# Performance work log

Hardware: AMD Instinct MI355X
Metric: run time of the kernel (lower is better)

The kernel has to match this reference:

```python
import jax, jax.numpy as jnp
import numpy as np

IN_OUT_DIM = 1024
HALF = IN_OUT_DIM // 2  # 512
MID = 4096
HIDDEN = 4
BATCH = 8192


def _mlp(h, Ws, bs):
    # Linear+ReLU for all but last layer, plain Linear at the end.
    for W, b in zip(Ws[:-1], bs[:-1]):
        h = jax.nn.relu(h @ W + b)
    return h @ Ws[-1] + bs[-1]


def setup_inputs() -> dict:
    key = jax.random.key(0)
    ks = jax.random.split(key, 16)
    inp = {
        "x": jax.random.normal(ks[0], (BATCH, IN_OUT_DIM), dtype=jnp.float32),
        "log_det_J": jnp.zeros((1,), dtype=jnp.float32),
    }
    dims = [HALF] + [MID] * (HIDDEN + 1) + [HALF]
    # Layers: 512->4096, (4096->4096) x4, 4096->512  => 6 Linear layers
    for i in range(len(dims) - 1):
        fan_in = dims[i]
        scale = 1.0 / np.sqrt(fan_in)
        inp[f"W{i}"] = jax.random.uniform(ks[1 + 2 * i], (dims[i], dims[i + 1]), jnp.float32, -scale, scale)
        inp[f"b{i}"] = jax.random.uniform(ks[2 + 2 * i], (dims[i + 1],), jnp.float32, -scale, scale)
    return inp


def reference(x, log_det_J, W0, b0, W1, b1, W2, b2, W3, b3, W4, b4, W5, b5):
    Ws = [W0, W1, W2, W3, W4, W5]
    bs = [b0, b1, b2, b3, b4, b5]
    # split_channels_even_odd: even cols 0,2,4..., odd cols 1,3,5...
    even = x[:, 0::2]  # [B, HALF]
    odd = x[:, 1::2]   # [B, HALF]
    # mask_config=1: transform even using MLP(odd), keep odd. reverse=False -> add.
    transformed = even + _mlp(odd, Ws, bs)
    kept = odd
    # stack_data with mask_config=1: columns [t0, k0, t1, k1, ...]
    B = x.shape[0]
    stacked = jnp.stack([transformed, kept], axis=2).reshape(B, -1)
    return stacked, log_det_J
```

## Files before the change

kernel.cpp:

```cpp
#include <hip/hip_runtime.h>
#include <hip/hip_bf16.h>
#include <hip/hip_fp16.h>


typedef __attribute__((ext_vector_type(8))) _Float16 f16x8;
typedef __attribute__((ext_vector_type(4))) float    f32x4;
typedef __attribute__((ext_vector_type(4))) int      i32x4;

#define B_ROWS 8192
#define D_HALF 512
#define D_MID  4096

__device__ __forceinline__ void gld_lds16(const void* gptr, void* lptr) {
    __builtin_amdgcn_global_load_lds(
        (const __attribute__((address_space(1))) void*)gptr,
        (__attribute__((address_space(3))) void*)lptr,
        16, 0, 0);
}

__device__ __forceinline__ void amax_commit(float m, int lane, float* amax_out) {
#pragma unroll
    for (int off = 32; off > 0; off >>= 1)
        m = fmaxf(m, __shfl_down(m, off));
    if (lane == 0) atomicMax((unsigned int*)amax_out, __float_as_uint(m));
}

__global__ __launch_bounds__(256) void transpose_convert_f16(
    const float* __restrict__ src, __half* __restrict__ dst, int K, int N)
{
    __shared__ float tile[32][33];
    const int kt = blockIdx.y * 32, nt = blockIdx.x * 32;
    const int tx = threadIdx.x, ty = threadIdx.y;
#pragma unroll
    for (int i = 0; i < 32; i += 8)
        tile[ty + i][tx] = src[(size_t)(kt + ty + i) * N + nt + tx];
    __syncthreads();
#pragma unroll
    for (int i = 0; i < 32; i += 8)
        dst[(size_t)(nt + ty + i) * K + kt + tx] = __float2half(tile[tx][ty + i]);
}

__global__ __launch_bounds__(256) void transpose_convert_i8(
    const float* __restrict__ src, signed char* __restrict__ dst, int K, int N)
{
    __shared__ float tile[32][33];
    const int kt = blockIdx.y * 32, nt = blockIdx.x * 32;
    const int tx = threadIdx.x, ty = threadIdx.y;
#pragma unroll
    for (int i = 0; i < 32; i += 8)
        tile[ty + i][tx] = src[(size_t)(kt + ty + i) * N + nt + tx];
    __syncthreads();
#pragma unroll
    for (int i = 0; i < 32; i += 8) {
        int q = __float2int_rn(tile[tx][ty + i] * 8128.0f);
        q = q > 127 ? 127 : (q < -127 ? -127 : q);
        dst[(size_t)(nt + ty + i) * K + kt + tx] = (signed char)q;
    }
}

__global__ __launch_bounds__(256) void extract_odd(
    const float* __restrict__ x, __half* __restrict__ odd,
    const float* __restrict__ ldj, float* __restrict__ out)
{
    const int idx = blockIdx.x * 256 + threadIdx.x;
    const float2 v = ((const float2*)x)[idx];
    odd[idx] = __float2half(v.y);
    if (idx == 0) out[(size_t)B_ROWS * 1024] = ldj[0];
}

__global__ __launch_bounds__(256) void quantize_i8(
    const __half* __restrict__ h, const float* __restrict__ amaxp,
    signed char* __restrict__ q)
{
    const int idx = blockIdx.x * 256 + threadIdx.x;
    const float inv = 127.0f / amaxp[0];
    const f16x8 v = ((const f16x8*)h)[idx];
    int p0 = 0, p1 = 0;
#pragma unroll
    for (int k = 0; k < 4; k++) {
        int a = __float2int_rn((float)v[k] * inv);
        a = a > 127 ? 127 : a;
        p0 |= a << (8 * k);
    }
#pragma unroll
    for (int k = 0; k < 4; k++) {
        int a = __float2int_rn((float)v[4 + k] * inv);
        a = a > 127 ? 127 : a;
        p1 |= a << (8 * k);
    }
    ((int2*)q)[idx] = make_int2(p0, p1);
}

template <int MODE>
__global__ __launch_bounds__(256, 2) void gemm_f16(
    const __half* __restrict__ A, const __half* __restrict__ Bt,
    const float* __restrict__ bias,
    __half* __restrict__ Ch, const float* __restrict__ xin,
    float* __restrict__ outp, float* __restrict__ amax_out,
    int M, int N, int K)
{
    __shared__ __half sA[128 * 32];
    __shared__ __half sB[128 * 32];

    const int tid  = threadIdx.x;
    const int wave = tid >> 6;
    const int lane = tid & 63;
    const int wm = wave >> 1, wn = wave & 1;
    const int quad = lane >> 4, l16 = lane & 15;
    const int bm = blockIdx.y, bn = blockIdx.x;

    const int    srow   = wave * 16 + (lane >> 2);
    const int    schunk = ((lane & 3) - ((lane >> 3) & 3)) & 3;
    const size_t ldb    = (size_t)K * 2;

    const char* Ag = (const char*)A  + (size_t)(bm * 128 + srow) * ldb + schunk * 16;
    const char* Bg = (const char*)Bt + (size_t)(bn * 128 + srow) * ldb + schunk * 16;
    char* sA0 = (char*)sA + wave * 16 * 64;
    char* sB0 = (char*)sB + wave * 16 * 64;

    const int pc = (quad + ((l16 >> 1) & 3)) & 3;
    const __half* aBase = sA + (wm * 64 + l16) * 32 + pc * 8;
    const __half* bBase = sB + (wn * 64 + l16) * 32 + pc * 8;

    f32x4 acc[4][4] = {};

    for (int k0 = 0; k0 < K; k0 += 32) {
        __syncthreads();
        const size_t kb = (size_t)k0 * 2;
        gld_lds16(Ag + kb,            sA0);
        gld_lds16(Ag + 64 * ldb + kb, sA0 + 64 * 64);
        gld_lds16(Bg + kb,            sB0);
        gld_lds16(Bg + 64 * ldb + kb, sB0 + 64 * 64);
        __syncthreads();

        f16x8 a[4], b[4];
#pragma unroll
        for (int i = 0; i < 4; i++) a[i] = *(const f16x8*)(aBase + i * 16 * 32);
#pragma unroll
        for (int j = 0; j < 4; j++) b[j] = *(const f16x8*)(bBase + j * 16 * 32);
#pragma unroll
        for (int i = 0; i < 4; i++)
#pragma unroll
            for (int j = 0; j < 4; j++)
                acc[i][j] = __builtin_amdgcn_mfma_f32_16x16x32_f16(a[i], b[j], acc[i][j], 0, 0, 0);
    }

    const int m0 = bm * 128 + wm * 64;
    const int n0 = bn * 128 + wn * 64;
    float lmax = 0.0f;
#pragma unroll
    for (int j = 0; j < 4; j++) {
        const int n  = n0 + j * 16 + l16;
        const float bv = bias[n];
#pragma unroll
        for (int i = 0; i < 4; i++) {
            const int mb = m0 + i * 16 + quad * 4;
#pragma unroll
            for (int r = 0; r < 4; r++) {
                float v = acc[i][j][r] + bv;
                if (MODE == 0) {
                    v = v > 0.0f ? v : 0.0f;
                    lmax = fmaxf(lmax, v);
                    Ch[(size_t)(mb + r) * N + n] = __float2half(v);
                } else {
                    const size_t p = (size_t)(mb + r) * 512 + n;
                    const float2 xv = ((const float2*)xin)[p];
                    float2 o; o.x = xv.x + v; o.y = xv.y;
                    ((float2*)outp)[p] = o;
                }
            }
        }
    }
    if (MODE == 0) amax_commit(lmax, lane, amax_out);
}

__global__ __launch_bounds__(512, 2) void gemm_i8_256(
    const signed char* __restrict__ A, const signed char* __restrict__ Bt,
    const float* __restrict__ bias, const float* __restrict__ amaxp,
    __half* __restrict__ Ch, float* __restrict__ amax_out,
    int M, int N, int K)
{
    __shared__ __align__(16) signed char lds[131072];

    const int tid  = threadIdx.x;
    const int wave = tid >> 6;
    const int lane = tid & 63;
    const int wm = wave >> 2, wn = wave & 3;
    const int quad = lane >> 4, l16 = lane & 15;
    const int bm = blockIdx.y, bn = blockIdx.x;

    const int srow   = tid >> 2;
    const int schunk = ((tid & 3) - ((tid >> 3) & 3)) & 3;
    const signed char* Ag = A  + (size_t)(bm * 256 + srow) * K + schunk * 16;
    const signed char* Bg = Bt + (size_t)(bn * 256 + srow) * K + schunk * 16;

    signed char* ldsA = lds;
    signed char* ldsB = lds + 65536;
    const int woff = wave * 1024;

    const int pc = (quad + ((l16 >> 1) & 3)) & 3;
    const signed char* aB = ldsA + (wm * 128 + l16) * 64 + pc * 16;
    const signed char* bB = ldsB + (wn * 64  + l16) * 64 + pc * 16;

    i32x4 acc[8][4] = {};
    const int NT = K >> 6;

#define STAGE_A(TT) { const size_t kb = (size_t)(TT) * 64;                       \
        signed char* d = ldsA + ((TT) & 3) * 16384 + woff;                        \
        gld_lds16(Ag + kb, d); gld_lds16(Ag + (size_t)128 * K + kb, d + 8192); }
#define STAGE_B(TT) { const size_t kb = (size_t)(TT) * 64;                       \
        signed char* d = ldsB + ((TT) & 3) * 16384 + woff;                        \
        gld_lds16(Bg + kb, d); gld_lds16(Bg + (size_t)128 * K + kb, d + 8192); }

    STAGE_A(0); STAGE_B(0);
    STAGE_A(1); STAGE_B(1);
    STAGE_A(2); STAGE_B(2);

    for (int t = 0; t < NT; ++t) {
        const signed char* aT = aB + (t & 3) * 16384;
        const signed char* bT = bB + (t & 3) * 16384;

        if (t < NT - 2)       asm volatile("s_waitcnt vmcnt(8)" ::: "memory");
        else if (t == NT - 2) asm volatile("s_waitcnt vmcnt(4)" ::: "memory");
        else                  asm volatile("s_waitcnt vmcnt(0)" ::: "memory");
        __builtin_amdgcn_s_barrier();

        i32x4 a[4], b[4];
#pragma unroll
        for (int j = 0; j < 4; j++) b[j] = *(const i32x4*)(bT + j * 16 * 64);
#pragma unroll
        for (int i = 0; i < 4; i++) a[i] = *(const i32x4*)(aT + i * 16 * 64);
        if (t + 3 < NT) STAGE_A(t + 3);
        __builtin_amdgcn_s_barrier();
        __builtin_amdgcn_s_setprio(1);
#pragma unroll
        for (int i = 0; i < 4; i++)
#pragma unroll
            for (int j = 0; j < 4; j++)
                acc[i][j] = __builtin_amdgcn_mfma_i32_16x16x64_i8(a[i], b[j], acc[i][j], 0, 0, 0);
        __builtin_amdgcn_s_setprio(0);
        __builtin_amdgcn_s_barrier();

#pragma unroll
        for (int i = 0; i < 4; i++) a[i] = *(const i32x4*)(aT + (4 + i) * 16 * 64);
        if (t + 3 < NT) STAGE_B(t + 3);
        __builtin_amdgcn_s_barrier();
        __builtin_amdgcn_s_setprio(1);
#pragma unroll
        for (int i = 0; i < 4; i++)
#pragma unroll
            for (int j = 0; j < 4; j++)
                acc[4 + i][j] = __builtin_amdgcn_mfma_i32_16x16x64_i8(a[i], b[j], acc[4 + i][j], 0, 0, 0);
        __builtin_amdgcn_s_setprio(0);
        __builtin_amdgcn_s_barrier();
    }
#undef STAGE_A
#undef STAGE_B

    const float sdq = amaxp[0] * (1.0f / (127.0f * 8128.0f));
    const int m0 = bm * 256 + wm * 128;
    const int n0 = bn * 256 + wn * 64;
    float lmax = 0.0f;
#pragma unroll
    for (int j = 0; j < 4; j++) {
        const int n  = n0 + j * 16 + l16;
        const float bv = bias[n];
#pragma unroll
        for (int i = 0; i < 8; i++) {
            const int mb = m0 + i * 16 + quad * 4;
#pragma unroll
            for (int r = 0; r < 4; r++) {
                float v = (float)acc[i][j][r] * sdq + bv;
                v = v > 0.0f ? v : 0.0f;
                lmax = fmaxf(lmax, v);
                Ch[(size_t)(mb + r) * N + n] = __float2half(v);
            }
        }
    }
    amax_commit(lmax, lane, amax_out);
}

extern "C" void kernel_launch(void* const* d_in, const int* in_sizes, int n_in,
                              void* d_out, int out_size, void* d_ws, size_t ws_size,
                              hipStream_t stream)
{
    const float* x   = (const float*)d_in[0];
    const float* ldj = (const float*)d_in[1];
    const float* W[6];
    const float* bb[6];
    for (int i = 0; i < 6; i++) {
        W[i]  = (const float*)d_in[2 + 2 * i];
        bb[i] = (const float*)d_in[3 + 2 * i];
    }
    float* out = (float*)d_out;

    char* ws = (char*)d_ws;
    size_t off = 0;
    float* amax = (float*)ws;                       off += 256;
    __half* Wt0 = (__half*)(ws + off);              off += (size_t)D_HALF * D_MID * 2;
    __half* Wt5 = (__half*)(ws + off);              off += (size_t)D_MID * D_HALF * 2;
    signed char* W8[4];
    for (int i = 0; i < 4; i++) { W8[i] = (signed char*)(ws + off); off += (size_t)D_MID * D_MID; }
    __half* hA = (__half*)(ws + off);               off += (size_t)B_ROWS * D_MID * 2;
    __half* hB = (__half*)(ws + off);               off += (size_t)B_ROWS * D_MID * 2;
    signed char* a8 = (signed char*)(ws + off);     off += (size_t)B_ROWS * D_MID;
    __half* odd = (__half*)(ws + off);              off += (size_t)B_ROWS * D_HALF * 2;

    hipMemsetAsync(amax, 0, 64, stream);

    {   dim3 g(D_MID / 32, D_HALF / 32), b(32, 8);
        transpose_convert_f16<<<g, b, 0, stream>>>(W[0], Wt0, D_HALF, D_MID); }
    for (int i = 1; i <= 4; i++) {
        dim3 g(D_MID / 32, D_MID / 32), b(32, 8);
        transpose_convert_i8<<<g, b, 0, stream>>>(W[i], W8[i - 1], D_MID, D_MID);
    }
    {   dim3 g(D_HALF / 32, D_MID / 32), b(32, 8);
        transpose_convert_f16<<<g, b, 0, stream>>>(W[5], Wt5, D_MID, D_HALF); }

    extract_odd<<<(B_ROWS * D_HALF) / 256, 256, 0, stream>>>(x, odd, ldj, out);

    const int QG = (B_ROWS * D_MID / 8) / 256;

    {   dim3 g(D_MID / 128, B_ROWS / 128);
        gemm_f16<0><<<g, 256, 0, stream>>>(odd, Wt0, bb[0], hA, nullptr, nullptr, amax + 0, B_ROWS, D_MID, D_HALF); }
    quantize_i8<<<QG, 256, 0, stream>>>(hA, amax + 0, a8);
    {   dim3 g(D_MID / 256, B_ROWS / 256);
        gemm_i8_256<<<g, 512, 0, stream>>>(a8, W8[0], bb[1], amax + 0, hB, amax + 1, B_ROWS, D_MID, D_MID); }
    quantize_i8<<<QG, 256, 0, stream>>>(hB, amax + 1, a8);
    {   dim3 g(D_MID / 256, B_ROWS / 256);
        gemm_i8_256<<<g, 512, 0, stream>>>(a8, W8[1], bb[2], amax + 1, hA, amax + 2, B_ROWS, D_MID, D_MID); }
    quantize_i8<<<QG, 256, 0, stream>>>(hA, amax + 2, a8);
    {   dim3 g(D_MID / 256, B_ROWS / 256);
        gemm_i8_256<<<g, 512, 0, stream>>>(a8, W8[2], bb[3], amax + 2, hB, amax + 3, B_ROWS, D_MID, D_MID); }
    quantize_i8<<<QG, 256, 0, stream>>>(hB, amax + 3, a8);
    {   dim3 g(D_MID / 256, B_ROWS / 256);
        gemm_i8_256<<<g, 512, 0, stream>>>(a8, W8[3], bb[4], amax + 3, hA, amax + 4, B_ROWS, D_MID, D_MID); }
    {   dim3 g(D_HALF / 128, B_ROWS / 128);
        gemm_f16<1><<<g, 256, 0, stream>>>(hA, Wt5, bb[5], nullptr, x, out, nullptr, B_ROWS, D_HALF, D_MID); }
}
```

Measured before the change: 1.260 ms.

## Restructure int8 GEMM main loop, add XCD block swizzle and LDS-staged epilogue

Remaps workgroup IDs so consecutive blocks land on the same XCD chunk, which should improve L2 reuse. The K loop now issues both the A and B prefetch loads at the top of each iteration and uses a single barrier-separated MFMA phase instead of two half-phases, cutting barriers per tile. The epilogue writes fp16 results to LDS and then issues 16-byte coalesced global stores instead of scattered 2-byte stores. The risks are higher register pressure from holding eight A fragments at once, and LDS reuse in the epilogue that relies on the final barrier.

```diff
diff --git a/kernel.cpp b/kernel.cpp
--- a/kernel.cpp
+++ b/kernel.cpp
@@ -187,7 +187,12 @@
     const int lane = tid & 63;
     const int wm = wave >> 2, wn = wave & 3;
     const int quad = lane >> 4, l16 = lane & 15;
-    const int bm = blockIdx.y, bn = blockIdx.x;
+
+    const int nwg  = gridDim.x * gridDim.y;
+    const int orig = blockIdx.y * gridDim.x + blockIdx.x;
+    const int swz  = (orig & 7) * (nwg >> 3) + (orig >> 3);
+    const int bn   = swz % gridDim.x;
+    const int bm   = swz / gridDim.x;
 
     const int srow   = tid >> 2;
     const int schunk = ((tid & 3) - ((tid >> 3) & 3)) & 3;
@@ -205,77 +210,73 @@
     i32x4 acc[8][4] = {};
     const int NT = K >> 6;
 
-#define STAGE_A(TT) { const size_t kb = (size_t)(TT) * 64;                       \
-        signed char* d = ldsA + ((TT) & 3) * 16384 + woff;                        \
-        gld_lds16(Ag + kb, d); gld_lds16(Ag + (size_t)128 * K + kb, d + 8192); }
-#define STAGE_B(TT) { const size_t kb = (size_t)(TT) * 64;                       \
-        signed char* d = ldsB + ((TT) & 3) * 16384 + woff;                        \
-        gld_lds16(Bg + kb, d); gld_lds16(Bg + (size_t)128 * K + kb, d + 8192); }
-
-    STAGE_A(0); STAGE_B(0);
-    STAGE_A(1); STAGE_B(1);
-    STAGE_A(2); STAGE_B(2);
+#define STAGE(TT) { const size_t kb = (size_t)(TT) * 64;                          \
+        signed char* dA = ldsA + ((TT) & 3) * 16384 + woff;                       \
+        signed char* dB = ldsB + ((TT) & 3) * 16384 + woff;                       \
+        gld_lds16(Ag + kb, dA); gld_lds16(Ag + (size_t)128 * K + kb, dA + 8192);  \
+        gld_lds16(Bg + kb, dB); gld_lds16(Bg + (size_t)128 * K + kb, dB + 8192); }
+
+    STAGE(0); STAGE(1); STAGE(2);
 
     for (int t = 0; t < NT; ++t) {
+        if (t + 3 < NT) { STAGE(t + 3);
+                          asm volatile("s_waitcnt vmcnt(12)" ::: "memory"); }
+        else if (t + 3 == NT) asm volatile("s_waitcnt vmcnt(8)"  ::: "memory");
+        else if (t + 2 == NT) asm volatile("s_waitcnt vmcnt(4)"  ::: "memory");
+        else                  asm volatile("s_waitcnt vmcnt(0)"  ::: "memory");
+        __builtin_amdgcn_s_barrier();
+
         const signed char* aT = aB + (t & 3) * 16384;
         const signed char* bT = bB + (t & 3) * 16384;
-
-        if (t < NT - 2)       asm volatile("s_waitcnt vmcnt(8)" ::: "memory");
-        else if (t == NT - 2) asm volatile("s_waitcnt vmcnt(4)" ::: "memory");
-        else                  asm volatile("s_waitcnt vmcnt(0)" ::: "memory");
-        __builtin_amdgcn_s_barrier();
-
-        i32x4 a[4], b[4];
-#pragma unroll
-        for (int j = 0; j < 4; j++) b[j] = *(const i32x4*)(bT + j * 16 * 64);
-#pragma unroll
-        for (int i = 0; i < 4; i++) a[i] = *(const i32x4*)(aT + i * 16 * 64);
-        if (t + 3 < NT) STAGE_A(t + 3);
-        __builtin_amdgcn_s_barrier();
+        i32x4 a0[4], a1[4], b[4];
+#pragma unroll
+        for (int j = 0; j < 4; j++) b[j]  = *(const i32x4*)(bT + j * 16 * 64);
+#pragma unroll
+        for (int i = 0; i < 4; i++) a0[i] = *(const i32x4*)(aT + i * 16 * 64);
+#pragma unroll
+        for (int i = 0; i < 4; i++) a1[i] = *(const i32x4*)(aT + (4 + i) * 16 * 64);
+
         __builtin_amdgcn_s_setprio(1);
 #pragma unroll
         for (int i = 0; i < 4; i++)
 #pragma unroll
             for (int j = 0; j < 4; j++)
-                acc[i][j] = __builtin_amdgcn_mfma_i32_16x16x64_i8(a[i], b[j], acc[i][j], 0, 0, 0);
+                acc[i][j] = __builtin_amdgcn_mfma_i32_16x16x64_i8(a0[i], b[j], acc[i][j], 0, 0, 0);
+#pragma unroll
+        for (int i = 0; i < 4; i++)
+#pragma unroll
+            for (int j = 0; j < 4; j++)
+                acc[4 + i][j] = __builtin_amdgcn_mfma_i32_16x16x64_i8(a1[i], b[j], acc[4 + i][j], 0, 0, 0);
         __builtin_amdgcn_s_setprio(0);
         __builtin_amdgcn_s_barrier();
-
-#pragma unroll
-        for (int i = 0; i < 4; i++) a[i] = *(const i32x4*)(aT + (4 + i) * 16 * 64);
-        if (t + 3 < NT) STAGE_B(t + 3);
-        __builtin_amdgcn_s_barrier();
-        __builtin_amdgcn_s_setprio(1);
-#pragma unroll
-        for (int i = 0; i < 4; i++)
-#pragma unroll
-            for (int j = 0; j < 4; j++)
-                acc[4 + i][j] = __builtin_amdgcn_mfma_i32_16x16x64_i8(a[i], b[j], acc[4 + i][j], 0, 0, 0);
-        __builtin_amdgcn_s_setprio(0);
-        __builtin_amdgcn_s_barrier();
-    }
-#undef STAGE_A
-#undef STAGE_B
+    }
+#undef STAGE
 
     const float sdq = amaxp[0] * (1.0f / (127.0f * 8128.0f));
-    const int m0 = bm * 256 + wm * 128;
     const int n0 = bn * 256 + wn * 64;
+    __half* lw = (__half*)(lds + wave * 16384);
     float lmax = 0.0f;
 #pragma unroll
     for (int j = 0; j < 4; j++) {
-        const int n  = n0 + j * 16 + l16;
-        const float bv = bias[n];
+        const float bv = bias[n0 + j * 16 + l16];
 #pragma unroll
         for (int i = 0; i < 8; i++) {
-            const int mb = m0 + i * 16 + quad * 4;
 #pragma unroll
             for (int r = 0; r < 4; r++) {
                 float v = (float)acc[i][j][r] * sdq + bv;
                 v = v > 0.0f ? v : 0.0f;
                 lmax = fmaxf(lmax, v);
-                Ch[(size_t)(mb + r) * N + n] = __float2half(v);
+                lw[(i * 16 + quad * 4 + r) * 64 + j * 16 + l16] = __float2half(v);
             }
         }
+    }
+    const int lrow0 = lane >> 3, c0 = (lane & 7) * 8;
+    const size_t gbase = (size_t)(bm * 256 + wm * 128) * N + n0 + c0;
+#pragma unroll
+    for (int p = 0; p < 16; p++) {
+        const int lr = p * 8 + lrow0;
+        f16x8 vv = *(const f16x8*)(lw + lr * 64 + c0);
+        *(f16x8*)(&Ch[gbase + (size_t)lr * N]) = vv;
     }
     amax_commit(lmax, lane, amax_out);
 }
```

Measured after the change: 1.268 ms. Within noise of the previous version (+0.6%).
